# Kernel tuning notes

Measured on AMD Instinct MI355X. Metric: run time of the kernel, lower is better.

Reference implementation:

```python
import jax, jax.numpy as jnp
import numpy as np

EPS = 1e-6
TEMPERATURE = 0.1
NEG_INF = -1.0e9

B, S, H = 8, 1024, 1024
M = 16384  # memory_size


def setup_inputs() -> dict:
    key = jax.random.key(0)
    ks = jax.random.split(key, 10)
    sc = 1.0 / np.sqrt(H)
    return {
        "hidden_states": jax.random.normal(ks[0], (B, S, H), jnp.float32),
        "Wk": jax.random.normal(ks[1], (H, H), jnp.float32) * sc,
        "bk": jax.random.normal(ks[2], (H,), jnp.float32) * 0.01,
        "Wv": jax.random.normal(ks[3], (H, H), jnp.float32) * sc,
        "bv": jax.random.normal(ks[4], (H,), jnp.float32) * 0.01,
        "Wo": jax.random.normal(ks[5], (H, H), jnp.float32) * sc,
        "bo": jax.random.normal(ks[6], (H,), jnp.float32) * 0.01,
        "memory_keys": jax.random.normal(ks[7], (M, H), jnp.float32),
        "memory_values": jax.random.normal(ks[8], (M, H), jnp.float32),
        "memory_usage": jax.random.randint(ks[9], (M,), 0, 3, jnp.int32),
    }


def _normalize(x):
    # matches torch: x * rsqrt(sum(x^2) + 1e-6)
    return x * jax.lax.rsqrt(jnp.sum(jnp.square(x), axis=-1, keepdims=True) + EPS)


def reference(hidden_states, Wk, bk, Wv, bv, Wo, bo,
              memory_keys, memory_values, memory_usage):
    # key projection + L2-ish normalization of queries
    q = hidden_states @ Wk.T + bk              # [B,S,H]
    qn = _normalize(q)
    mkn = _normalize(memory_keys)              # [M,H]
    # cosine-similarity attention over memory slots
    scores = jnp.einsum('bsh,mh->bsm', qn, mkn) / TEMPERATURE  # [B,S,M]
    mask = (memory_usage > 0).astype(scores.dtype)             # [M]
    scores = scores * mask + NEG_INF * (1.0 - mask)
    w = jax.nn.softmax(scores, axis=-1)                        # [B,S,M]
    retrieved = jnp.einsum('bsm,mh->bsh', w, memory_values)    # [B,S,H]
    return retrieved @ Wo.T + bo
```

## Files before the change

### kernel.cpp

```cpp
#include <hip/hip_runtime.h>
#include <hip/hip_bf16.h>
#include <stdint.h>
#include <stddef.h>

typedef __bf16 bf16_t;
typedef __attribute__((ext_vector_type(8))) __bf16 bf16x8;
typedef __attribute__((ext_vector_type(4))) __bf16 bf16x4;
typedef __attribute__((ext_vector_type(4))) float f32x4;

#define HDIM 1024
#define MSLOTS 16384
#define NROWS 8192

__device__ __forceinline__ void load16_lds(const void* g, void* l) {
  __builtin_amdgcn_global_load_lds((const __attribute__((address_space(1))) void*)g,
                                   (__attribute__((address_space(3))) void*)l, 16, 0, 0);
}

__global__ void init_compact(int* __restrict__ cmask) {
  int i = blockIdx.x * blockDim.x + threadIdx.x;
  if (i < MSLOTS) cmask[i] = 0;
}

__global__ void compact_scan(const int* __restrict__ usage, int* __restrict__ posmap,
                             int* __restrict__ cmask, int* __restrict__ smalls) {
  __shared__ int wtot[16], wbase[16];
  const int t = threadIdx.x;
  const int lane = t & 63, wid = t >> 6;
  const int base = t * 16;
  unsigned mask = 0;
  int c = 0;
  #pragma unroll
  for (int i = 0; i < 16; ++i) {
    if (usage[base + i] > 0) { mask |= (1u << i); ++c; }
  }
  int inc = c;
  #pragma unroll
  for (int d = 1; d < 64; d <<= 1) {
    int n = __shfl_up(inc, d);
    if (lane >= d) inc += n;
  }
  if (lane == 63) wtot[wid] = inc;
  __syncthreads();
  if (t == 0) {
    int acc = 0;
    #pragma unroll
    for (int w = 0; w < 16; ++w) { wbase[w] = acc; acc += wtot[w]; }
    smalls[0] = acc;
    smalls[1] = ((acc + 511) >> 9) << 9;
  }
  __syncthreads();
  int pos = wbase[wid] + inc - c;
  #pragma unroll
  for (int i = 0; i < 16; ++i) {
    if ((mask >> i) & 1u) {
      posmap[pos] = base + i;
      cmask[pos] = 1;
      ++pos;
    }
  }
}

__global__ void cvt_f32_bf16(const float* __restrict__ X, bf16_t* __restrict__ Y, int n8) {
  int i = blockIdx.x * blockDim.x + threadIdx.x;
  if (i >= n8) return;
  float4 a = ((const float4*)X)[2 * i];
  float4 b = ((const float4*)X)[2 * i + 1];
  bf16x8 o;
  o[0] = (bf16_t)a.x; o[1] = (bf16_t)a.y; o[2] = (bf16_t)a.z; o[3] = (bf16_t)a.w;
  o[4] = (bf16_t)b.x; o[5] = (bf16_t)b.y; o[6] = (bf16_t)b.z; o[7] = (bf16_t)b.w;
  ((bf16x8*)Y)[i] = o;
}

__global__ void normalize_rows(const float* __restrict__ X, bf16_t* __restrict__ Y) {
  __shared__ float part[4];
  const int t = threadIdx.x;
  const size_t row = blockIdx.x;
  float4 v = ((const float4*)(X + row * 1024))[t];
  float s = v.x * v.x + v.y * v.y + v.z * v.z + v.w * v.w;
  #pragma unroll
  for (int m = 32; m >= 1; m >>= 1) s += __shfl_xor(s, m);
  if ((t & 63) == 0) part[t >> 6] = s;
  __syncthreads();
  float tot = part[0] + part[1] + part[2] + part[3];
  float r = rsqrtf(tot + 1e-6f);
  bf16x4 o;
  o[0] = (bf16_t)(v.x * r); o[1] = (bf16_t)(v.y * r);
  o[2] = (bf16_t)(v.z * r); o[3] = (bf16_t)(v.w * r);
  *(bf16x4*)&Y[row * 1024 + t * 4] = o;
}

__global__ void normalize_gather(const float* __restrict__ mk, const int* __restrict__ posmap,
                                 const int* __restrict__ smalls, bf16_t* __restrict__ cmkn) {
  __shared__ float part[4];
  const int p = blockIdx.x;
  const int cnt = smalls[0], mpad = smalls[1];
  if (p >= mpad) return;
  const int t = threadIdx.x;
  if (p >= cnt) {
    bf16x4 z;
    z[0] = z[1] = z[2] = z[3] = (bf16_t)0.f;
    *(bf16x4*)&cmkn[(size_t)p * 1024 + t * 4] = z;
    return;
  }
  const int slot = posmap[p];
  float4 v = ((const float4*)(mk + (size_t)slot * 1024))[t];
  float s = v.x * v.x + v.y * v.y + v.z * v.z + v.w * v.w;
  #pragma unroll
  for (int m = 32; m >= 1; m >>= 1) s += __shfl_xor(s, m);
  if ((t & 63) == 0) part[t >> 6] = s;
  __syncthreads();
  float tot = part[0] + part[1] + part[2] + part[3];
  float r = rsqrtf(tot + 1e-6f);
  bf16x4 o;
  o[0] = (bf16_t)(v.x * r); o[1] = (bf16_t)(v.y * r);
  o[2] = (bf16_t)(v.z * r); o[3] = (bf16_t)(v.w * r);
  *(bf16x4*)&cmkn[(size_t)p * 1024 + t * 4] = o;
}

__global__ void transpose_gather(const float* __restrict__ mv, const int* __restrict__ posmap,
                                 const int* __restrict__ smalls, bf16_t* __restrict__ cVt) {
  __shared__ float tile[32][33];
  const int cnt = smalls[0], mpad = smalls[1];
  const int p0 = blockIdx.y * 32;
  if (p0 >= mpad) return;
  const int tx = threadIdx.x & 31, ty = threadIdx.x >> 5;
  const int h0 = blockIdx.x * 32;
  #pragma unroll
  for (int j = 0; j < 32; j += 8) {
    const int pos = p0 + ty + j;
    float val = 0.f;
    if (pos < cnt) val = mv[(size_t)posmap[pos] * 1024 + h0 + tx];
    tile[ty + j][tx] = val;
  }
  __syncthreads();
  #pragma unroll
  for (int j = 0; j < 32; j += 8)
    cVt[(size_t)(h0 + ty + j) * MSLOTS + p0 + tx] = (bf16_t)tile[tx][ty + j];
}

__global__ void zero_f32(float* __restrict__ p, int n4) {
  int i = blockIdx.x * blockDim.x + threadIdx.x;
  if (i < n4) ((float4*)p)[i] = (float4){0.f, 0.f, 0.f, 0.f};
}

__global__ void scale_cvt(const float* __restrict__ retrf, const float* __restrict__ den,
                          bf16_t* __restrict__ out, int n4) {
  int i = blockIdx.x * blockDim.x + threadIdx.x;
  if (i >= n4) return;
  float4 s = ((const float4*)retrf)[i];
  const int row = (i * 4) >> 10;
  const float r = 1.0f / den[row];
  bf16x4 o;
  o[0] = (bf16_t)(s.x * r); o[1] = (bf16_t)(s.y * r);
  o[2] = (bf16_t)(s.z * r); o[3] = (bf16_t)(s.w * r);
  ((bf16x4*)out)[i] = o;
}

__global__ void reduce_scale(const float* __restrict__ part, size_t partStride, int ks,
                             const float* __restrict__ den, bf16_t* __restrict__ out, int n4) {
  int i = blockIdx.x * blockDim.x + threadIdx.x;
  if (i >= n4) return;
  float4 s = ((const float4*)part)[i];
  for (int k = 1; k < ks; ++k) {
    float4 t = ((const float4*)(part + (size_t)k * partStride))[i];
    s.x += t.x; s.y += t.y; s.z += t.z; s.w += t.w;
  }
  const int row = (i * 4) >> 10;
  const float r = 1.0f / den[row];
  bf16x4 o;
  o[0] = (bf16_t)(s.x * r); o[1] = (bf16_t)(s.y * r);
  o[2] = (bf16_t)(s.z * r); o[3] = (bf16_t)(s.w * r);
  ((bf16x4*)out)[i] = o;
}

#define SB __builtin_amdgcn_sched_barrier(0)

#define STAGE(TT, HF)                                                          \
  {                                                                            \
    const int isB_ = ((HF) < 2) ? 1 : 0;                                       \
    const int h_ = (HF) & 1;                                                   \
    bf16_t* d_ = &sm[(TT) & 1][isB_][h_ * 8192 + tid * 8];                     \
    const bf16_t* s_ = (isB_ ? pBstg : pAstg) + (size_t)h_ * 128 * ldk +       \
                       (size_t)(kstart + ((TT) << 6));                         \
    load16_lds(s_, d_);                                                        \
    load16_lds(s_ + (size_t)64 * ldk, d_ + 4096);                              \
  }

#define RDA(Q)                                                                 \
  {                                                                            \
    _Pragma("unroll") for (int m2 = 0; m2 < 2; ++m2)                           \
      _Pragma("unroll") for (int kk = 0; kk < 2; ++kk) {                       \
        const int r_ = (Q) * 64 + wr * 32 + m2 * 16 + lr;                      \
        const int sg_ = kk * 4 + lq;                                           \
        af[m2 * 2 + kk] =                                                      \
            *(const bf16x8*)(bA + r_ * 128 + ((sg_ ^ (r_ & 7)) << 4));         \
      }                                                                        \
  }

#define RDB()                                                                  \
  {                                                                            \
    _Pragma("unroll") for (int n = 0; n < 4; ++n)                              \
      _Pragma("unroll") for (int kk = 0; kk < 2; ++kk) {                       \
        const int r_ = wc * 64 + n * 16 + lr;                                  \
        const int sg_ = kk * 4 + lq;                                           \
        bfr[n * 2 + kk] =                                                      \
            *(const bf16x8*)(bB + r_ * 128 + ((sg_ ^ (r_ & 7)) << 4));         \
      }                                                                        \
  }

#define MFQ(Q)                                                                 \
  {                                                                            \
    _Pragma("unroll") for (int m2 = 0; m2 < 2; ++m2)                           \
      _Pragma("unroll") for (int n = 0; n < 4; ++n)                            \
        _Pragma("unroll") for (int kk = 0; kk < 2; ++kk)                       \
          acc[(Q) * 2 + m2][n] = __builtin_amdgcn_mfma_f32_16x16x32_bf16(      \
              af[m2 * 2 + kk], bfr[n * 2 + kk], acc[(Q) * 2 + m2][n], 0, 0, 0);\
  }

template <int EPI>
__global__ __launch_bounds__(512, 2)
void gemm256(const bf16_t* __restrict__ A, const bf16_t* __restrict__ Bt,
             int ldk, int kLenIn, int ldc,
             const int* __restrict__ cmask,
             float* __restrict__ den,
             float* __restrict__ outf, bf16_t* __restrict__ outb,
             const int* __restrict__ smalls, int ks, size_t partStride) {
  __shared__ bf16_t sm[2][2][256 * 64];
  const int tid = threadIdx.x;
  const int lane = tid & 63;
  const int wave = tid >> 6;
  const int wr = wave >> 2;
  const int wc = wave & 3;
  const int lr = lane & 15;
  const int lq = lane >> 4;

  int bx = blockIdx.x, by = blockIdx.y, bz = blockIdx.z;
  {
    const unsigned nx = gridDim.x, ny = gridDim.y;
    if ((ny & 7u) == 0u) {
      unsigned lin = blockIdx.x + nx * (blockIdx.y + ny * blockIdx.z);
      unsigned ylow = lin & 7u;
      lin >>= 3;
      const unsigned nyh = ny >> 3;
      unsigned yhigh = lin % nyh;
      lin /= nyh;
      bx = lin % nx;
      bz = lin / nx;
      by = ylow + 8u * yhigh;
    }
  }

  int kLen = kLenIn;
  int kstart = 0;
  if (EPI == 1) {
    if (bx * 256 >= smalls[1]) return;
  }
  if (EPI == 3 || EPI == 4) {
    kLen = smalls[1] / ks;
    kstart = bz * kLen;
  }
  const int nt = kLen >> 6;
  if (nt <= 0) return;

  const size_t stgOff = (size_t)(tid >> 3) * ldk + (((tid & 7) ^ ((tid >> 3) & 7)) << 3);
  const bf16_t* pAstg = A + (size_t)(by * 256) * ldk + stgOff;
  const bf16_t* pBstg = Bt + (size_t)(bx * 256) * ldk + stgOff;

  f32x4 acc[8][4];
  #pragma unroll
  for (int m = 0; m < 8; ++m)
    #pragma unroll
    for (int n = 0; n < 4; ++n) acc[m][n] = (f32x4){0.f, 0.f, 0.f, 0.f};

  bf16x8 af[4], bfr[8];

  STAGE(0, 0); STAGE(0, 1); STAGE(0, 2); STAGE(0, 3);

  for (int t = 0; t < nt; ++t) {
    const char* bA = (const char*)sm[t & 1][0];
    const char* bB = (const char*)sm[t & 1][1];
    const bool more = (t + 1 < nt);

    asm volatile("s_waitcnt vmcnt(2)" ::: "memory");
    SB; __builtin_amdgcn_s_barrier(); SB;
    if (more) STAGE(t + 1, 0);
    RDB();
    RDA(0);
    __builtin_amdgcn_s_setprio(1); MFQ(0); __builtin_amdgcn_s_setprio(0); SB;

    __builtin_amdgcn_s_barrier(); SB;
    if (more) STAGE(t + 1, 1);
    RDA(1);
    __builtin_amdgcn_s_setprio(1); MFQ(1); __builtin_amdgcn_s_setprio(0); SB;

    if (more) { asm volatile("s_waitcnt vmcnt(4)" ::: "memory"); }
    else      { asm volatile("s_waitcnt vmcnt(0)" ::: "memory"); }
    SB; __builtin_amdgcn_s_barrier(); SB;
    if (more) STAGE(t + 1, 2);
    RDA(2);
    __builtin_amdgcn_s_setprio(1); MFQ(2); __builtin_amdgcn_s_setprio(0); SB;

    __builtin_amdgcn_s_barrier(); SB;
    if (more) STAGE(t + 1, 3);
    RDA(3);
    __builtin_amdgcn_s_setprio(1); MFQ(3); __builtin_amdgcn_s_setprio(0); SB;
  }

  const int colBase = bx * 256 + wc * 64 + lr;

  if (EPI == 1) {
    bool ok[4];
    #pragma unroll
    for (int n = 0; n < 4; ++n) ok[n] = cmask[colBase + n * 16] > 0;
    #pragma unroll
    for (int m = 0; m < 8; ++m) {
      const int row0 = by * 256 + (m >> 1) * 64 + wr * 32 + (m & 1) * 16 + lq * 4;
      #pragma unroll
      for (int r = 0; r < 4; ++r) {
        const int row = row0 + r;
        float s = 0.f;
        #pragma unroll
        for (int n = 0; n < 4; ++n) {
          float e = ok[n] ? exp2f(acc[m][n][r] * 14.426950408889634f) : 0.f;
          s += e;
          outb[(size_t)row * ldc + colBase + n * 16] = (bf16_t)e;
        }
        s += __shfl_xor(s, 1);
        s += __shfl_xor(s, 2);
        s += __shfl_xor(s, 4);
        s += __shfl_xor(s, 8);
        if (lr == 0) atomicAdd(&den[row], s);
      }
    }
  }
  if (EPI == 3 || EPI == 4) {
    if (EPI == 4) outf += (size_t)bz * partStride;
    #pragma unroll
    for (int m = 0; m < 8; ++m) {
      const int row0 = by * 256 + (m >> 1) * 64 + wr * 32 + (m & 1) * 16 + lq * 4;
      #pragma unroll
      for (int n = 0; n < 4; ++n)
        #pragma unroll
        for (int r = 0; r < 4; ++r) {
          const size_t idx = (size_t)(row0 + r) * ldc + colBase + n * 16;
          if (EPI == 3) atomicAdd(&outf[idx], acc[m][n][r]);
          else outf[idx] = acc[m][n][r];
        }
    }
  }
}

__global__ void gemm_bt(const bf16_t* __restrict__ A, const bf16_t* __restrict__ Bt,
                        int ldk, int kLenIn, int ldc,
                        const float* __restrict__ bias,
                        float* __restrict__ outf) {
  __shared__ bf16_t lA[128 * 32];
  __shared__ bf16_t lB[128 * 32];
  const int t = threadIdx.x;
  const int lane = t & 63;
  const int wave = t >> 6;
  const int wm = (wave >> 1) << 6;
  const int wn = (wave & 1) << 6;
  const int lr = lane & 15;
  const int lq = lane >> 4;

  int bx = blockIdx.x, by = blockIdx.y;
  {
    const unsigned nx = gridDim.x, ny = gridDim.y;
    if ((ny & 7u) == 0u) {
      unsigned lin = blockIdx.x + nx * blockIdx.y;
      unsigned ylow = lin & 7u;
      lin >>= 3;
      const unsigned nyh = ny >> 3;
      unsigned yhigh = lin % nyh;
      lin /= nyh;
      bx = lin % nx;
      by = ylow + 8u * yhigh;
    }
  }

  const int kLen = kLenIn;
  const int r0 = t >> 2;
  const int c0 = (t & 3) * 8;
  const bf16_t* pA0 = A + (size_t)(by * 128 + r0) * ldk + c0;
  const bf16_t* pA1 = pA0 + (size_t)64 * ldk;
  const bf16_t* pB0 = Bt + (size_t)(bx * 128 + r0) * ldk + c0;
  const bf16_t* pB1 = pB0 + (size_t)64 * ldk;

  f32x4 acc[4][4];
  #pragma unroll
  for (int i = 0; i < 4; ++i)
    #pragma unroll
    for (int j = 0; j < 4; ++j) acc[i][j] = (f32x4){0.f, 0.f, 0.f, 0.f};

  for (int k0 = 0; k0 < kLen; k0 += 32) {
    __syncthreads();
    load16_lds(pA0, &lA[t * 8]);
    load16_lds(pA1, &lA[2048 + t * 8]);
    load16_lds(pB0, &lB[t * 8]);
    load16_lds(pB1, &lB[2048 + t * 8]);
    pA0 += 32; pA1 += 32; pB0 += 32; pB1 += 32;
    __syncthreads();
    bf16x8 af[4], bfv[4];
    #pragma unroll
    for (int i = 0; i < 4; ++i)
      af[i] = *(const bf16x8*)&lA[(wm + i * 16 + lr) * 32 + lq * 8];
    #pragma unroll
    for (int j = 0; j < 4; ++j)
      bfv[j] = *(const bf16x8*)&lB[(wn + j * 16 + lr) * 32 + lq * 8];
    #pragma unroll
    for (int i = 0; i < 4; ++i)
      #pragma unroll
      for (int j = 0; j < 4; ++j)
        acc[i][j] = __builtin_amdgcn_mfma_f32_16x16x32_bf16(af[i], bfv[j], acc[i][j], 0, 0, 0);
  }

  const int colBase = bx * 128 + wn + lr;
  const int rowBase = by * 128 + wm + lq * 4;

  #pragma unroll
  for (int j = 0; j < 4; ++j) {
    const int col = colBase + j * 16;
    const float bval = bias[col];
    #pragma unroll
    for (int i = 0; i < 4; ++i) {
      const int row = rowBase + i * 16;
      #pragma unroll
      for (int r = 0; r < 4; ++r)
        outf[(size_t)(row + r) * ldc + col] = acc[i][j][r] + bval;
    }
  }
}

extern "C" void kernel_launch(void* const* d_in, const int* in_sizes, int n_in,
                              void* d_out, int out_size, void* d_ws, size_t ws_size,
                              hipStream_t stream) {
  const float* hs = (const float*)d_in[0];
  const float* Wk = (const float*)d_in[1];
  const float* bk = (const float*)d_in[2];
  const float* Wo = (const float*)d_in[5];
  const float* bo = (const float*)d_in[6];
  const float* mk = (const float*)d_in[7];
  const float* mv = (const float*)d_in[8];
  const int* usage = (const int*)d_in[9];
  float* out = (float*)d_out;

  char* ws = (char*)d_ws;
  size_t off = 0;
  auto alloc = [&](size_t b) -> void* {
    void* p = ws + off;
    off += (b + 255) & ~(size_t)255;
    return p;
  };
  bf16_t* cmkn = (bf16_t*)alloc((size_t)MSLOTS * HDIM * 2);
  bf16_t* cVt = (bf16_t*)alloc((size_t)HDIM * MSLOTS * 2);
  bf16_t* qnb = (bf16_t*)alloc((size_t)NROWS * HDIM * 2);
  bf16_t* retrb = (bf16_t*)alloc((size_t)NROWS * HDIM * 2);
  bf16_t* Wob = (bf16_t*)alloc((size_t)HDIM * HDIM * 2);
  float* den = (float*)alloc((size_t)NROWS * 4);
  int* posmap = (int*)alloc((size_t)MSLOTS * 4);
  int* cmask = (int*)alloc((size_t)MSLOTS * 4);
  int* smalls = (int*)alloc(256 * 4);
  const size_t fixed = off;

  int chunk = 256, ksplit = 4, partialMode = 0;
  {
    const int cc[8] = {4096, 4096, 2048, 2048, 1024, 1024, 512, 256};
    const int kk[8] = {4, 4, 8, 8, 8, 8, 8, 4};
    const int pp[8] = {1, 0, 1, 0, 1, 0, 0, 0};
    for (int ci = 0; ci < 8; ++ci) {
      size_t outBytes = pp[ci] ? (size_t)cc[ci] * HDIM * 4 * kk[ci] : (size_t)cc[ci] * HDIM * 4;
      size_t region = (size_t)cc[ci] * MSLOTS * 2 + outBytes;
      size_t phaseA = (size_t)NROWS * HDIM * 2 + (size_t)HDIM * HDIM * 2 +
                      (size_t)NROWS * HDIM * 4 + 1024;
      if (region < phaseA) region = phaseA;
      if (fixed + region <= ws_size) {
        chunk = cc[ci]; ksplit = kk[ci]; partialMode = pp[ci];
        break;
      }
    }
  }
  bf16_t* hsb = (bf16_t*)(ws + fixed);
  bf16_t* Wkb = (bf16_t*)(ws + fixed + (size_t)NROWS * HDIM * 2);
  float* qf = (float*)(ws + fixed + (size_t)NROWS * HDIM * 2 + (size_t)HDIM * HDIM * 2);
  bf16_t* P = (bf16_t*)(ws + fixed);
  float* retrf = (float*)(ws + fixed + (size_t)chunk * MSLOTS * 2);
  const size_t partStride = (size_t)chunk * HDIM;

  init_compact<<<MSLOTS / 256, 256, 0, stream>>>(cmask);
  compact_scan<<<1, 1024, 0, stream>>>(usage, posmap, cmask, smalls);
  cvt_f32_bf16<<<(NROWS * HDIM / 8 + 255) / 256, 256, 0, stream>>>(hs, hsb, NROWS * HDIM / 8);
  cvt_f32_bf16<<<(HDIM * HDIM / 8 + 255) / 256, 256, 0, stream>>>(Wk, Wkb, HDIM * HDIM / 8);
  cvt_f32_bf16<<<(HDIM * HDIM / 8 + 255) / 256, 256, 0, stream>>>(Wo, Wob, HDIM * HDIM / 8);
  normalize_gather<<<MSLOTS, 256, 0, stream>>>(mk, posmap, smalls, cmkn);
  transpose_gather<<<dim3(HDIM / 32, MSLOTS / 32), 256, 0, stream>>>(mv, posmap, smalls, cVt);

  gemm_bt<<<dim3(HDIM / 128, NROWS / 128), 256, 0, stream>>>(
      hsb, Wkb, HDIM, HDIM, HDIM, bk, qf);
  normalize_rows<<<NROWS, 256, 0, stream>>>(qf, qnb);

  for (int c = 0; c < NROWS; c += chunk) {
    zero_f32<<<(chunk / 4 + 255) / 256, 256, 0, stream>>>(den, chunk / 4);
    gemm256<1><<<dim3(MSLOTS / 256, chunk / 256), 512, 0, stream>>>(
        qnb + (size_t)c * HDIM, cmkn, HDIM, HDIM, MSLOTS, cmask, den, nullptr, P,
        smalls, 1, 0);
    if (partialMode) {
      gemm256<4><<<dim3(HDIM / 256, chunk / 256, ksplit), 512, 0, stream>>>(
          P, cVt, MSLOTS, 0, HDIM, nullptr, nullptr, retrf, nullptr, smalls, ksplit,
          partStride);
      reduce_scale<<<(chunk * HDIM / 4 + 255) / 256, 256, 0, stream>>>(
          retrf, partStride, ksplit, den, retrb + (size_t)c * HDIM, chunk * HDIM / 4);
    } else {
      zero_f32<<<(chunk * HDIM / 4 + 255) / 256, 256, 0, stream>>>(retrf, chunk * HDIM / 4);
      gemm256<3><<<dim3(HDIM / 256, chunk / 256, ksplit), 512, 0, stream>>>(
          P, cVt, MSLOTS, 0, HDIM, nullptr, nullptr, retrf, nullptr, smalls, ksplit,
          0);
      scale_cvt<<<(chunk * HDIM / 4 + 255) / 256, 256, 0, stream>>>(
          retrf, den, retrb + (size_t)c * HDIM, chunk * HDIM / 4);
    }
  }

  gemm_bt<<<dim3(HDIM / 128, NROWS / 128), 256, 0, stream>>>(
      retrb, Wob, HDIM, HDIM, HDIM, bo, out);
}
```

Before: 796.7 us.

## Reschedule GEMM main loop with barriers bracketing each MFMA phase

```diff
diff --git a/kernel.cpp b/kernel.cpp
--- a/kernel.cpp
+++ b/kernel.cpp
@@ -217,6 +217,11 @@
           acc[(Q) * 2 + m2][n] = __builtin_amdgcn_mfma_f32_16x16x32_bf16(      \
               af[m2 * 2 + kk], bfr[n * 2 + kk], acc[(Q) * 2 + m2][n], 0, 0, 0);\
   }
+
+#define MFMA_PHASE(Q)                                                          \
+  __builtin_amdgcn_s_barrier(); SB;                                            \
+  __builtin_amdgcn_s_setprio(1); MFQ(Q); __builtin_amdgcn_s_setprio(0);        \
+  SB; __builtin_amdgcn_s_barrier(); SB;
 
 template <int EPI>
 __global__ __launch_bounds__(512, 2)
@@ -276,35 +281,42 @@
   bf16x8 af[4], bfr[8];
 
   STAGE(0, 0); STAGE(0, 1); STAGE(0, 2); STAGE(0, 3);
+  asm volatile("s_waitcnt vmcnt(2)" ::: "memory");
+  SB; __builtin_amdgcn_s_barrier(); SB;
 
   for (int t = 0; t < nt; ++t) {
     const char* bA = (const char*)sm[t & 1][0];
     const char* bB = (const char*)sm[t & 1][1];
     const bool more = (t + 1 < nt);
 
-    asm volatile("s_waitcnt vmcnt(2)" ::: "memory");
-    SB; __builtin_amdgcn_s_barrier(); SB;
-    if (more) STAGE(t + 1, 0);
     RDB();
     RDA(0);
-    __builtin_amdgcn_s_setprio(1); MFQ(0); __builtin_amdgcn_s_setprio(0); SB;
-
-    __builtin_amdgcn_s_barrier(); SB;
-    if (more) STAGE(t + 1, 1);
+    if (more) STAGE(t + 1, 0);
+    SB;
+    MFMA_PHASE(0);
+
     RDA(1);
-    __builtin_amdgcn_s_setprio(1); MFQ(1); __builtin_amdgcn_s_setprio(0); SB;
-
-    if (more) { asm volatile("s_waitcnt vmcnt(4)" ::: "memory"); }
-    else      { asm volatile("s_waitcnt vmcnt(0)" ::: "memory"); }
-    SB; __builtin_amdgcn_s_barrier(); SB;
+    if (more) {
+      STAGE(t + 1, 1);
+      asm volatile("s_waitcnt vmcnt(4)" ::: "memory");
+    } else {
+      asm volatile("s_waitcnt vmcnt(0)" ::: "memory");
+    }
+    SB;
+    MFMA_PHASE(1);
+
+    RDA(2);
     if (more) STAGE(t + 1, 2);
-    RDA(2);
-    __builtin_amdgcn_s_setprio(1); MFQ(2); __builtin_amdgcn_s_setprio(0); SB;
-
-    __builtin_amdgcn_s_barrier(); SB;
-    if (more) STAGE(t + 1, 3);
+    SB;
+    MFMA_PHASE(2);
+
     RDA(3);
-    __builtin_amdgcn_s_setprio(1); MFQ(3); __builtin_amdgcn_s_setprio(0); SB;
+    if (more) {
+      STAGE(t + 1, 3);
+      asm volatile("s_waitcnt vmcnt(2)" ::: "memory");
+    }
+    SB;
+    MFMA_PHASE(3);
   }
 
   const int colBase = bx * 256 + wc * 64 + lr;
```

Measured after the change: 800.6 us. About the same (+0.5%).
